# Performance work log

Measured on AMD Instinct MI355X. Metric: run time of the kernel, lower is better.

Reference implementation:

```python
import jax, jax.numpy as jnp
import numpy as np

B = 8192
N_INPUTS = 16 * 12 * 64  # 12288, FEATURE_FACTORIZE=False
H0, H1, H2 = 256, 32, 32
OUTPUT_SCALE = 300.0
WDL_SCALE = 200.0
AVG_ACTIVE = 30.0  # ~30 active features per position (NNUE sparsity)


def setup_inputs() -> dict:
    key = jax.random.key(0)
    ks = jax.random.split(key, 11)
    p = AVG_ACTIVE / N_INPUTS
    # near-one-hot sparse binary feature vectors, as produced by get_features()
    wf = (jax.random.uniform(ks[0], (B, N_INPUTS)) < p).astype(jnp.float32)
    bf = (jax.random.uniform(ks[1], (B, N_INPUTS)) < p).astype(jnp.float32)
    side = jax.random.randint(ks[2], (B,), 0, 2).astype(jnp.bool_)
    qs1, qs2, qs3 = float(1 << 6), float(1 << 6), float(1 << 5)
    ft_w = jax.random.normal(ks[3], (H0, N_INPUTS), jnp.float32) * jnp.sqrt(2.0 / N_INPUTS)
    ft_b = jax.random.normal(ks[4], (H0,), jnp.float32) * 0.5
    l1_w = jax.random.normal(ks[5], (H1, 2 * H0), jnp.float32) * (32.0 / qs1)
    l1_b = jax.random.normal(ks[6], (H1,), jnp.float32) * 0.5
    l2_w = jax.random.normal(ks[7], (H2, H1), jnp.float32) * (32.0 / qs2)
    l2_b = jax.random.normal(ks[8], (H2,), jnp.float32) * 0.5
    l3_w = jax.random.normal(ks[9], (1, H2), jnp.float32) * (2048.0 / (OUTPUT_SCALE * qs3))
    l3_b = jax.random.normal(ks[10], (1,), jnp.float32) * 0.5
    return {"white_features": wf, "black_features": bf, "side": side,
            "ft_w": ft_w, "ft_b": ft_b, "l1_w": l1_w, "l1_b": l1_b,
            "l2_w": l2_w, "l2_b": l2_b, "l3_w": l3_w, "l3_b": l3_b}


def reference(white_features, black_features, side, ft_w, ft_b,
              l1_w, l1_b, l2_w, l2_b, l3_w, l3_b):
    # feature transformer on each perspective: [B, H0]
    w = white_features @ ft_w.T + ft_b
    b = black_features @ ft_w.T + ft_b
    s = side[:, None]
    # side-to-move perspective first: [B, 2*H0]
    acc = jnp.where(s, jnp.concatenate([w, b], axis=1),
                    jnp.concatenate([b, w], axis=1))
    o0 = jnp.clip(acc, 0.0, 1.0)
    o1 = jnp.clip(o0 @ l1_w.T + l1_b, 0.0, 1.0)
    o2 = jnp.clip(o1 @ l2_w.T + l2_b, 0.0, 1.0)
    o3 = (o2 @ l3_w.T + l3_b) * OUTPUT_SCALE  # [B, 1]
    return jax.nn.sigmoid(o3 / WDL_SCALE)
```

## Files before the change

### kernel.cpp

```cpp
#include <hip/hip_runtime.h>
#include <math.h>

#define NB 8192
#define NI 12288
#define H0 256
#define H1 32
#define H2 32
#define MAXA 256
#define OUT_SCALE 300.0f
#define WDL_SCALE 200.0f

typedef float f32x4 __attribute__((ext_vector_type(4)));

__global__ __launch_bounds__(256) void nnue_ft_transpose(
    const float* __restrict__ src, float* __restrict__ dst)
{
    __shared__ float tile[64][65];
    const int bx = blockIdx.x;
    const int by = blockIdx.y;
    const int tx = threadIdx.x;
    const int ty = threadIdx.y;
    const int col = bx * 64 + tx;
    for (int j = ty; j < 64; j += 4)
        tile[j][tx] = src[(size_t)(by * 64 + j) * NI + col];
    __syncthreads();
    const int h = by * 64 + tx;
    for (int j = ty; j < 64; j += 4)
        dst[(size_t)(bx * 64 + j) * H0 + h] = tile[tx][j];
}

__global__ __launch_bounds__(256) void nnue_fwd(
    const float* __restrict__ wf, const float* __restrict__ bf,
    const int* __restrict__ side,
    const float* __restrict__ ft,
    const float* __restrict__ ft_b,
    const float* __restrict__ l1_w, const float* __restrict__ l1_b,
    const float* __restrict__ l2_w, const float* __restrict__ l2_b,
    const float* __restrict__ l3_w, const float* __restrict__ l3_b,
    float* __restrict__ out, int tflag)
{
    __shared__ int   idxW[MAXA], idxB[MAXA];
    __shared__ int   cnts[2];
    __shared__ float pacc[4][2][H0] __attribute__((aligned(16)));
    __shared__ float o0[2 * H0];
    __shared__ float o1[H1];

    const int row = blockIdx.x;
    const int t   = threadIdx.x;
    if (t < 2) cnts[t] = 0;
    __syncthreads();

    const f32x4* wf4 = (const f32x4*)(wf + (size_t)row * NI);
    const f32x4* bf4 = (const f32x4*)(bf + (size_t)row * NI);
    const float ftb = ft_b[t];

    {
        f32x4 v[12];
        #pragma unroll
        for (int k = 0; k < 12; ++k)
            v[k] = __builtin_nontemporal_load(&wf4[t + k * 256]);
        #pragma unroll
        for (int k = 0; k < 12; ++k) {
            const int base = (t + k * 256) * 4;
            int m = (v[k].x != 0.f ? 1 : 0) | (v[k].y != 0.f ? 2 : 0)
                  | (v[k].z != 0.f ? 4 : 0) | (v[k].w != 0.f ? 8 : 0);
            while (m) {
                const int b = __ffs(m) - 1;
                m &= m - 1;
                idxW[atomicAdd(&cnts[0], 1)] = base + b;
            }
        }
    }
    {
        f32x4 v[12];
        #pragma unroll
        for (int k = 0; k < 12; ++k)
            v[k] = __builtin_nontemporal_load(&bf4[t + k * 256]);
        #pragma unroll
        for (int k = 0; k < 12; ++k) {
            const int base = (t + k * 256) * 4;
            int m = (v[k].x != 0.f ? 1 : 0) | (v[k].y != 0.f ? 2 : 0)
                  | (v[k].z != 0.f ? 4 : 0) | (v[k].w != 0.f ? 8 : 0);
            while (m) {
                const int b = __ffs(m) - 1;
                m &= m - 1;
                idxB[atomicAdd(&cnts[1], 1)] = base + b;
            }
        }
    }
    __syncthreads();

    const int nW = cnts[0], nB = cnts[1];
    const int w = t >> 6;
    const int l = t & 63;

    if (tflag) {
        f32x4 aw0 = {0.f, 0.f, 0.f, 0.f}, aw1 = {0.f, 0.f, 0.f, 0.f};
        int i = w;
        for (; i + 4 < nW; i += 8) {
            const f32x4 r0 = *(const f32x4*)(ft + (size_t)idxW[i] * H0 + 4 * l);
            const f32x4 r1 = *(const f32x4*)(ft + (size_t)idxW[i + 4] * H0 + 4 * l);
            aw0 += r0; aw1 += r1;
        }
        if (i < nW)
            aw0 += *(const f32x4*)(ft + (size_t)idxW[i] * H0 + 4 * l);

        f32x4 ab0 = {0.f, 0.f, 0.f, 0.f}, ab1 = {0.f, 0.f, 0.f, 0.f};
        i = w;
        for (; i + 4 < nB; i += 8) {
            const f32x4 r0 = *(const f32x4*)(ft + (size_t)idxB[i] * H0 + 4 * l);
            const f32x4 r1 = *(const f32x4*)(ft + (size_t)idxB[i + 4] * H0 + 4 * l);
            ab0 += r0; ab1 += r1;
        }
        if (i < nB)
            ab0 += *(const f32x4*)(ft + (size_t)idxB[i] * H0 + 4 * l);

        *(f32x4*)&pacc[w][0][4 * l] = aw0 + aw1;
        *(f32x4*)&pacc[w][1][4 * l] = ab0 + ab1;
    } else {
        float aW = 0.f, aB = 0.f;
        const float* ftr = ft + (size_t)t * NI;
        for (int j = 0; j < nW; ++j) aW += ftr[idxW[j]];
        for (int j = 0; j < nB; ++j) aB += ftr[idxB[j]];
        if (w == 0) { pacc[0][0][t % 64] = 0.f; }
        pacc[0][0][t] = aW; pacc[1][0][t] = 0.f; pacc[2][0][t] = 0.f; pacc[3][0][t] = 0.f;
        pacc[0][1][t] = aB; pacc[1][1][t] = 0.f; pacc[2][1][t] = 0.f; pacc[3][1][t] = 0.f;
    }
    __syncthreads();

    const float accW = ftb + ((pacc[0][0][t] + pacc[1][0][t]) + (pacc[2][0][t] + pacc[3][0][t]));
    const float accB = ftb + ((pacc[0][1][t] + pacc[1][1][t]) + (pacc[2][1][t] + pacc[3][1][t]));
    const bool s = side[row] != 0;
    const float wv = fminf(fmaxf(accW, 0.f), 1.f);
    const float bv = fminf(fmaxf(accB, 0.f), 1.f);
    o0[t]      = s ? wv : bv;
    o0[t + H0] = s ? bv : wv;
    __syncthreads();

    {
        const int j = t >> 3, p = t & 7;
        const float* wrow = l1_w + j * (2 * H0);
        float sum = 0.f;
        #pragma unroll
        for (int m = 0; m < 64; ++m) {
            const int k = p + 8 * m;
            sum += wrow[k] * o0[k];
        }
        sum += __shfl_xor(sum, 1);
        sum += __shfl_xor(sum, 2);
        sum += __shfl_xor(sum, 4);
        if (p == 0) o1[j] = fminf(fmaxf(sum + l1_b[j], 0.f), 1.f);
    }
    __syncthreads();

    if (t < 32) {
        const float* wrow = l2_w + t * H1;
        float sum2 = 0.f;
        #pragma unroll
        for (int k = 0; k < H1; ++k) sum2 += wrow[k] * o1[k];
        const float o2v = fminf(fmaxf(sum2 + l2_b[t], 0.f), 1.f);
        float part = o2v * l3_w[t];
        part += __shfl_xor(part, 1);
        part += __shfl_xor(part, 2);
        part += __shfl_xor(part, 4);
        part += __shfl_xor(part, 8);
        part += __shfl_xor(part, 16);
        if (t == 0) {
            const float o3 = (part + l3_b[0]) * OUT_SCALE;
            out[row] = 1.f / (1.f + __expf(-o3 / WDL_SCALE));
        }
    }
}

extern "C" void kernel_launch(void* const* d_in, const int* in_sizes, int n_in,
                              void* d_out, int out_size, void* d_ws, size_t ws_size,
                              hipStream_t stream) {
    const float* wf   = (const float*)d_in[0];
    const float* bf   = (const float*)d_in[1];
    const int*   side = (const int*)d_in[2];
    const float* ft_w = (const float*)d_in[3];
    const float* ft_b = (const float*)d_in[4];
    const float* l1_w = (const float*)d_in[5];
    const float* l1_b = (const float*)d_in[6];
    const float* l2_w = (const float*)d_in[7];
    const float* l2_b = (const float*)d_in[8];
    const float* l3_w = (const float*)d_in[9];
    const float* l3_b = (const float*)d_in[10];
    float*       out  = (float*)d_out;

    const size_t needT = (size_t)NI * H0 * sizeof(float);
    const int tflag = (ws_size >= needT) ? 1 : 0;
    const float* ft = ft_w;
    if (tflag) {
        float* ftT = (float*)d_ws;
        nnue_ft_transpose<<<dim3(NI / 64, H0 / 64), dim3(64, 4), 0, stream>>>(ft_w, ftT);
        ft = ftT;
    }
    nnue_fwd<<<NB, 256, 0, stream>>>(wf, bf, side, ft, ft_b,
                                     l1_w, l1_b, l2_w, l2_b, l3_w, l3_b,
                                     out, tflag);
}
```

Baseline: 177.3 us.

## Split sparse feature scan into separate kernel with global index lists

```diff
diff --git a/kernel.cpp b/kernel.cpp
--- a/kernel.cpp
+++ b/kernel.cpp
@@ -12,6 +12,17 @@
 
 typedef float f32x4 __attribute__((ext_vector_type(4)));
 
+#define FTT_B  ((size_t)NI * H0 * 4)
+#define CNT_B  ((size_t)2 * NB * 4)
+#define IDX_B  ((size_t)2 * NB * MAXA * 4)
+#define WS_NEED (FTT_B + CNT_B + IDX_B)
+
+__global__ __launch_bounds__(256) void nnue_zero_cnt(int* __restrict__ cnt)
+{
+    const int i = blockIdx.x * 256 + threadIdx.x;
+    if (i < 2 * NB) cnt[i] = 0;
+}
+
 __global__ __launch_bounds__(256) void nnue_ft_transpose(
     const float* __restrict__ src, float* __restrict__ dst)
 {
@@ -29,7 +40,140 @@
         dst[(size_t)(bx * 64 + j) * H0 + h] = tile[tx][j];
 }
 
-__global__ __launch_bounds__(256) void nnue_fwd(
+__global__ __launch_bounds__(256) void nnue_scan(
+    const float* __restrict__ wf, const float* __restrict__ bf,
+    int* __restrict__ cnt, int* __restrict__ idx)
+{
+    const int t     = threadIdx.x;
+    const int bid   = blockIdx.x;
+    const int persp = blockIdx.y;
+    const float* src = persp ? bf : wf;
+    int* mycnt = cnt + persp * NB;
+    int* myidx = idx + (size_t)persp * NB * MAXA;
+
+    const f32x4* s4 = (const f32x4*)src + (size_t)bid * 12288;
+    #pragma unroll 1
+    for (int it = 0; it < 6; ++it) {
+        f32x4 v[8];
+        #pragma unroll
+        for (int u = 0; u < 8; ++u)
+            v[u] = __builtin_nontemporal_load(&s4[it * 2048 + u * 256 + t]);
+        #pragma unroll
+        for (int u = 0; u < 8; ++u) {
+            int m = (v[u].x != 0.f ? 1 : 0) | (v[u].y != 0.f ? 2 : 0)
+                  | (v[u].z != 0.f ? 4 : 0) | (v[u].w != 0.f ? 8 : 0);
+            if (m) {
+                const int local = it * 2048 + u * 256 + t;
+                const int row_l = local / 3072;
+                const int pos   = (local - row_l * 3072) * 4;
+                const int row   = bid * 4 + row_l;
+                while (m) {
+                    const int b = __ffs(m) - 1;
+                    m &= m - 1;
+                    const int off = atomicAdd(&mycnt[row], 1);
+                    if (off < MAXA)
+                        myidx[(size_t)row * MAXA + off] = pos + b;
+                }
+            }
+        }
+    }
+}
+
+__global__ __launch_bounds__(256) void nnue_fwd2(
+    const int* __restrict__ cnt, const int* __restrict__ idx,
+    const int* __restrict__ side,
+    const float* __restrict__ ft,
+    const float* __restrict__ ft_b,
+    const float* __restrict__ l1_w, const float* __restrict__ l1_b,
+    const float* __restrict__ l2_w, const float* __restrict__ l2_b,
+    const float* __restrict__ l3_w, const float* __restrict__ l3_b,
+    float* __restrict__ out)
+{
+    __shared__ int   idxW[MAXA], idxB[MAXA];
+    __shared__ float pacc[4][2][H0] __attribute__((aligned(16)));
+    __shared__ float o0[2 * H0];
+    __shared__ float o1[H1];
+
+    const int row = blockIdx.x;
+    const int t   = threadIdx.x;
+    const int nW  = min(cnt[row], MAXA);
+    const int nB  = min(cnt[NB + row], MAXA);
+
+    idxW[t] = idx[(size_t)row * MAXA + t];
+    idxB[t] = idx[(size_t)(NB + row) * MAXA + t];
+    __syncthreads();
+
+    const int w = t >> 6, l = t & 63;
+    f32x4 aw0 = {0.f, 0.f, 0.f, 0.f}, aw1 = {0.f, 0.f, 0.f, 0.f};
+    int i = w;
+    for (; i + 4 < nW; i += 8) {
+        const f32x4 r0 = *(const f32x4*)(ft + (size_t)idxW[i] * H0 + 4 * l);
+        const f32x4 r1 = *(const f32x4*)(ft + (size_t)idxW[i + 4] * H0 + 4 * l);
+        aw0 += r0; aw1 += r1;
+    }
+    if (i < nW)
+        aw0 += *(const f32x4*)(ft + (size_t)idxW[i] * H0 + 4 * l);
+
+    f32x4 ab0 = {0.f, 0.f, 0.f, 0.f}, ab1 = {0.f, 0.f, 0.f, 0.f};
+    i = w;
+    for (; i + 4 < nB; i += 8) {
+        const f32x4 r0 = *(const f32x4*)(ft + (size_t)idxB[i] * H0 + 4 * l);
+        const f32x4 r1 = *(const f32x4*)(ft + (size_t)idxB[i + 4] * H0 + 4 * l);
+        ab0 += r0; ab1 += r1;
+    }
+    if (i < nB)
+        ab0 += *(const f32x4*)(ft + (size_t)idxB[i] * H0 + 4 * l);
+
+    *(f32x4*)&pacc[w][0][4 * l] = aw0 + aw1;
+    *(f32x4*)&pacc[w][1][4 * l] = ab0 + ab1;
+    __syncthreads();
+
+    const float ftb  = ft_b[t];
+    const float accW = ftb + ((pacc[0][0][t] + pacc[1][0][t]) + (pacc[2][0][t] + pacc[3][0][t]));
+    const float accB = ftb + ((pacc[0][1][t] + pacc[1][1][t]) + (pacc[2][1][t] + pacc[3][1][t]));
+    const bool s = side[row] != 0;
+    const float wv = fminf(fmaxf(accW, 0.f), 1.f);
+    const float bv = fminf(fmaxf(accB, 0.f), 1.f);
+    o0[t]      = s ? wv : bv;
+    o0[t + H0] = s ? bv : wv;
+    __syncthreads();
+
+    {
+        const int j = t >> 3, p = t & 7;
+        const float* wrow = l1_w + j * (2 * H0);
+        float sum = 0.f;
+        #pragma unroll
+        for (int m = 0; m < 64; ++m) {
+            const int k = p + 8 * m;
+            sum += wrow[k] * o0[k];
+        }
+        sum += __shfl_xor(sum, 1);
+        sum += __shfl_xor(sum, 2);
+        sum += __shfl_xor(sum, 4);
+        if (p == 0) o1[j] = fminf(fmaxf(sum + l1_b[j], 0.f), 1.f);
+    }
+    __syncthreads();
+
+    if (t < 32) {
+        const float* wrow = l2_w + t * H1;
+        float sum2 = 0.f;
+        #pragma unroll
+        for (int k = 0; k < H1; ++k) sum2 += wrow[k] * o1[k];
+        const float o2v = fminf(fmaxf(sum2 + l2_b[t], 0.f), 1.f);
+        float part = o2v * l3_w[t];
+        part += __shfl_xor(part, 1);
+        part += __shfl_xor(part, 2);
+        part += __shfl_xor(part, 4);
+        part += __shfl_xor(part, 8);
+        part += __shfl_xor(part, 16);
+        if (t == 0) {
+            const float o3 = (part + l3_b[0]) * OUT_SCALE;
+            out[row] = 1.f / (1.f + __expf(-o3 / WDL_SCALE));
+        }
+    }
+}
+
+__global__ __launch_bounds__(256) void nnue_fused_fallback(
     const float* __restrict__ wf, const float* __restrict__ bf,
     const int* __restrict__ side,
     const float* __restrict__ ft,
@@ -37,11 +181,10 @@
     const float* __restrict__ l1_w, const float* __restrict__ l1_b,
     const float* __restrict__ l2_w, const float* __restrict__ l2_b,
     const float* __restrict__ l3_w, const float* __restrict__ l3_b,
-    float* __restrict__ out, int tflag)
+    float* __restrict__ out)
 {
     __shared__ int   idxW[MAXA], idxB[MAXA];
     __shared__ int   cnts[2];
-    __shared__ float pacc[4][2][H0] __attribute__((aligned(16)));
     __shared__ float o0[2 * H0];
     __shared__ float o1[H1];
 
@@ -54,11 +197,13 @@
     const f32x4* bf4 = (const f32x4*)(bf + (size_t)row * NI);
     const float ftb = ft_b[t];
 
-    {
+    for (int half = 0; half < 2; ++half) {
+        const f32x4* p4 = half ? bf4 : wf4;
+        int* lst = half ? idxB : idxW;
         f32x4 v[12];
         #pragma unroll
         for (int k = 0; k < 12; ++k)
-            v[k] = __builtin_nontemporal_load(&wf4[t + k * 256]);
+            v[k] = __builtin_nontemporal_load(&p4[t + k * 256]);
         #pragma unroll
         for (int k = 0; k < 12; ++k) {
             const int base = (t + k * 256) * 4;
@@ -67,69 +212,18 @@
             while (m) {
                 const int b = __ffs(m) - 1;
                 m &= m - 1;
-                idxW[atomicAdd(&cnts[0], 1)] = base + b;
+                lst[atomicAdd(&cnts[half], 1)] = base + b;
             }
         }
     }
-    {
-        f32x4 v[12];
-        #pragma unroll
-        for (int k = 0; k < 12; ++k)
-            v[k] = __builtin_nontemporal_load(&bf4[t + k * 256]);
-        #pragma unroll
-        for (int k = 0; k < 12; ++k) {
-            const int base = (t + k * 256) * 4;
-            int m = (v[k].x != 0.f ? 1 : 0) | (v[k].y != 0.f ? 2 : 0)
-                  | (v[k].z != 0.f ? 4 : 0) | (v[k].w != 0.f ? 8 : 0);
-            while (m) {
-                const int b = __ffs(m) - 1;
-                m &= m - 1;
-                idxB[atomicAdd(&cnts[1], 1)] = base + b;
-            }
-        }
-    }
     __syncthreads();
 
     const int nW = cnts[0], nB = cnts[1];
-    const int w = t >> 6;
-    const int l = t & 63;
-
-    if (tflag) {
-        f32x4 aw0 = {0.f, 0.f, 0.f, 0.f}, aw1 = {0.f, 0.f, 0.f, 0.f};
-        int i = w;
-        for (; i + 4 < nW; i += 8) {
-            const f32x4 r0 = *(const f32x4*)(ft + (size_t)idxW[i] * H0 + 4 * l);
-            const f32x4 r1 = *(const f32x4*)(ft + (size_t)idxW[i + 4] * H0 + 4 * l);
-            aw0 += r0; aw1 += r1;
-        }
-        if (i < nW)
-            aw0 += *(const f32x4*)(ft + (size_t)idxW[i] * H0 + 4 * l);
-
-        f32x4 ab0 = {0.f, 0.f, 0.f, 0.f}, ab1 = {0.f, 0.f, 0.f, 0.f};
-        i = w;
-        for (; i + 4 < nB; i += 8) {
-            const f32x4 r0 = *(const f32x4*)(ft + (size_t)idxB[i] * H0 + 4 * l);
-            const f32x4 r1 = *(const f32x4*)(ft + (size_t)idxB[i + 4] * H0 + 4 * l);
-            ab0 += r0; ab1 += r1;
-        }
-        if (i < nB)
-            ab0 += *(const f32x4*)(ft + (size_t)idxB[i] * H0 + 4 * l);
-
-        *(f32x4*)&pacc[w][0][4 * l] = aw0 + aw1;
-        *(f32x4*)&pacc[w][1][4 * l] = ab0 + ab1;
-    } else {
-        float aW = 0.f, aB = 0.f;
-        const float* ftr = ft + (size_t)t * NI;
-        for (int j = 0; j < nW; ++j) aW += ftr[idxW[j]];
-        for (int j = 0; j < nB; ++j) aB += ftr[idxB[j]];
-        if (w == 0) { pacc[0][0][t % 64] = 0.f; }
-        pacc[0][0][t] = aW; pacc[1][0][t] = 0.f; pacc[2][0][t] = 0.f; pacc[3][0][t] = 0.f;
-        pacc[0][1][t] = aB; pacc[1][1][t] = 0.f; pacc[2][1][t] = 0.f; pacc[3][1][t] = 0.f;
-    }
-    __syncthreads();
-
-    const float accW = ftb + ((pacc[0][0][t] + pacc[1][0][t]) + (pacc[2][0][t] + pacc[3][0][t]));
-    const float accB = ftb + ((pacc[0][1][t] + pacc[1][1][t]) + (pacc[2][1][t] + pacc[3][1][t]));
+    float accW = ftb, accB = ftb;
+    const float* ftr = ft + (size_t)t * NI;
+    for (int j = 0; j < nW; ++j) accW += ftr[idxW[j]];
+    for (int j = 0; j < nB; ++j) accB += ftr[idxB[j]];
+
     const bool s = side[row] != 0;
     const float wv = fminf(fmaxf(accW, 0.f), 1.f);
     const float bv = fminf(fmaxf(accB, 0.f), 1.f);
@@ -142,10 +236,7 @@
         const float* wrow = l1_w + j * (2 * H0);
         float sum = 0.f;
         #pragma unroll
-        for (int m = 0; m < 64; ++m) {
-            const int k = p + 8 * m;
-            sum += wrow[k] * o0[k];
-        }
+        for (int m = 0; m < 64; ++m) sum += wrow[p + 8 * m] * o0[p + 8 * m];
         sum += __shfl_xor(sum, 1);
         sum += __shfl_xor(sum, 2);
         sum += __shfl_xor(sum, 4);
@@ -188,15 +279,19 @@
     const float* l3_b = (const float*)d_in[10];
     float*       out  = (float*)d_out;
 
-    const size_t needT = (size_t)NI * H0 * sizeof(float);
-    const int tflag = (ws_size >= needT) ? 1 : 0;
-    const float* ft = ft_w;
-    if (tflag) {
+    if (ws_size >= WS_NEED) {
         float* ftT = (float*)d_ws;
+        int*   cnt = (int*)((char*)d_ws + FTT_B);
+        int*   idx = (int*)((char*)d_ws + FTT_B + CNT_B);
+
+        nnue_zero_cnt<<<(2 * NB + 255) / 256, 256, 0, stream>>>(cnt);
+        nnue_scan<<<dim3(NB / 4, 2), 256, 0, stream>>>(wf, bf, cnt, idx);
         nnue_ft_transpose<<<dim3(NI / 64, H0 / 64), dim3(64, 4), 0, stream>>>(ft_w, ftT);
-        ft = ftT;
-    }
-    nnue_fwd<<<NB, 256, 0, stream>>>(wf, bf, side, ft, ft_b,
-                                     l1_w, l1_b, l2_w, l2_b, l3_w, l3_b,
-                                     out, tflag);
-}
+        nnue_fwd2<<<NB, 256, 0, stream>>>(cnt, idx, side, ftT, ft_b,
+                                          l1_w, l1_b, l2_w, l2_b, l3_w, l3_b, out);
+    } else {
+        nnue_fused_fallback<<<NB, 256, 0, stream>>>(wf, bf, side, ft_w, ft_b,
+                                                    l1_w, l1_b, l2_w, l2_b,
+                                                    l3_w, l3_b, out);
+    }
+}
```

New measurement: 230.6 us. 30.1% more time.
